# Optimization experiments

Measured on AMD Instinct MI355X. Metric: run time of the kernel, lower is better.

Reference implementation:

```python
import jax, jax.numpy as jnp
import numpy as np

SHAPE = 64
K = 8
HID = 512
OUT = K + 2 * K * SHAPE + 2 * SHAPE  # 1160
B, T = 32, 2048


def setup_inputs() -> dict:
    key = jax.random.key(0)
    ks = jax.random.split(key, 4)
    x = jax.random.normal(ks[0], (B, T, SHAPE), dtype=jnp.float32)
    W1 = jax.random.normal(ks[1], (SHAPE, HID), dtype=jnp.float32) / np.sqrt(SHAPE)
    b1 = jnp.zeros((HID,), dtype=jnp.float32)
    W2 = jax.random.normal(ks[2], (HID, HID), dtype=jnp.float32) / np.sqrt(HID)
    b2 = jnp.zeros((HID,), dtype=jnp.float32)
    W3 = jax.random.normal(ks[3], (HID, OUT), dtype=jnp.float32) / np.sqrt(HID) * 0.1
    b3 = jnp.zeros((OUT,), dtype=jnp.float32)
    return {"x": x, "W1": W1, "b1": b1, "W2": W2, "b2": b2, "W3": W3, "b3": b3}


def _coupling_forward(x, W1, b1, W2, b2, W3, b3):
    # coupling mask over feature dim: first half conditions the second half
    mask = jnp.zeros((SHAPE,), dtype=x.dtype).at[:SHAPE // 2].set(1.0)  # [D]
    x_ = x * mask  # [B,T,D]

    # conditioner MLP
    h = jax.nn.relu(x_ @ W1 + b1)
    h = jax.nn.relu(h @ W2 + b2)
    params = h @ W3 + b3  # [B,T,OUT]

    logscales = params[..., :SHAPE]
    biases = params[..., SHAPE:2 * SHAPE]
    mdn = params[..., 2 * SHAPE:]
    logits = mdn[..., :K]                                   # [B,T,K]
    mu = mdn[..., K:K + K * SHAPE].reshape(*x.shape[:2], K, SHAPE)
    logstd = mdn[..., K + K * SHAPE:].reshape(*x.shape[:2], K, SHAPE)

    # --- MixtureCDFFlow.flow ---
    weights = jax.nn.softmax(logits, axis=-1)[..., None]    # [B,T,K,1]
    std = jnp.exp(logstd)
    u = (x[:, :, None, :] - mu) / std                       # [B,T,K,D]
    cdf = 0.5 * (1.0 + jax.lax.erf(u / np.sqrt(2.0)))
    z = jnp.sum(cdf * weights, axis=2)                      # [B,T,D]
    pdf = jnp.exp(-0.5 * u * u) / (std * np.sqrt(2.0 * np.pi))
    logd_mix = jnp.log(jnp.sum(pdf * weights, axis=2))      # [B,T,D]

    # --- Inverse(Sigmoid).flow == Sigmoid.invert ---
    xs = -jnp.log(1.0 / z - 1.0)
    logd_sig = -jnp.log(z) - jnp.log(1.0 - z)

    # --- ElemwiseAffine.flow ---
    out = xs * jnp.exp(logscales) + biases
    log_det = logd_mix + logd_sig + logscales

    x_out = (1.0 - mask) * out + x_
    log_det = log_det * (1.0 - mask)
    return x_out, log_det


def reference(x, W1, b1, W2, b2, W3, b3):
    return _coupling_forward(x, W1, b1, W2, b2, W3, b3)
```

## Files before the change

kernel.cpp:

```cpp
#include <hip/hip_runtime.h>

typedef short short8 __attribute__((ext_vector_type(8)));
typedef float f32x4 __attribute__((ext_vector_type(4)));
typedef float f32x4v __attribute__((ext_vector_type(4)));

#define NROWS 65536
#define NCOMPACT 640

__device__ __forceinline__ short f2bf(float f) {
  union { float f; unsigned u; } c; c.f = f;
  unsigned r = (c.u + 0x7fffu + ((c.u >> 16) & 1u)) >> 16;
  return (short)r;
}

__device__ __forceinline__ float fastrcp(float a) {
  float r; asm("v_rcp_f32 %0, %1" : "=v"(r) : "v"(a)); return r;
}

__device__ __forceinline__ int w3col(int n) {
  if (n < 32)  return 32 + n;
  if (n < 64)  return 96 + (n - 32);
  if (n < 72)  return 128 + (n - 64);
  if (n < 96)  return -1;
  if (n < 352) { int q = n - 96;  return 168 + (q >> 5) * 64 + (q & 31); }
  if (n < 608) { int q = n - 352; return 680 + (q >> 5) * 64 + (q & 31); }
  return -1;
}

__global__ __launch_bounds__(256) void prep_w_kernel(
    const float* __restrict__ W1, const float* __restrict__ W2,
    const float* __restrict__ W3, const float* __restrict__ b3,
    short* __restrict__ w1t, short* __restrict__ w2t,
    short* __restrict__ w3t, float* __restrict__ b3c) {
  const int NW1 = 512 * 32, NW2 = 512 * 512, NW3 = NCOMPACT * 512;
  int t = blockIdx.x * 256 + threadIdx.x;
  if (t < NW1) {
    int n = t >> 5, k = t & 31;
    w1t[t] = f2bf(W1[k * 512 + n]);
  } else if (t < NW1 + NW2) {
    int i = t - NW1; int n = i >> 9, k = i & 511;
    w2t[i] = f2bf(W2[k * 512 + n]);
  } else if (t < NW1 + NW2 + NW3) {
    int i = t - NW1 - NW2; int n = i >> 9, k = i & 511;
    int c = w3col(n);
    w3t[i] = (c >= 0) ? f2bf(W3[(size_t)k * 1160 + c]) : (short)0;
  } else if (t < NW1 + NW2 + NW3 + NCOMPACT) {
    int n = t - NW1 - NW2 - NW3;
    int c = w3col(n);
    b3c[n] = (c >= 0) ? b3[c] : 0.0f;
  }
}

#define OFF_A 0
#define OFF_B 4096
#define OFF_C 45056
#define OFF_H 86016
#define PSTR 644

__global__ __launch_bounds__(1024) void mega_kernel(
    const float* __restrict__ x,
    const short* __restrict__ w1t,
    const float* __restrict__ b1,
    const short* __restrict__ w2t,
    const float* __restrict__ b2,
    const short* __restrict__ w3t,
    const float* __restrict__ b3c,
    float* __restrict__ out) {
  __shared__ __attribute__((aligned(16))) char lds[151552];
  const int tid = threadIdx.x;
  const int m0 = blockIdx.x * 64;
  const int lane = tid & 63, wid = tid >> 6;
  const int wr = wid >> 3, wc = wid & 7;
  const int lr = lane & 15, hi = lane >> 4, lk = hi * 8;
  short* Hs = (short*)(lds + OFF_H);

  auto STAGE_W = [&](int bo, const short* src, int stride, int kt, int nchunk) {
    for (int base = wid * 64; base < nchunk; base += 1024) {
      int c = base + lane;
      int row = c >> 2;
      int skb = ((c & 3) ^ ((row >> 1) & 3)) << 4;
      const char* g = (const char*)(src + (size_t)row * stride + kt) + skb;
      __builtin_amdgcn_global_load_lds(
          (const __attribute__((address_space(1))) void*)g,
          (__attribute__((address_space(3))) void*)(lds + bo + (size_t)base * 16),
          16, 0, 0);
    }
  };

  if (tid < 256) {
    int row = tid >> 2, seg = tid & 3;
    const float* src = x + (size_t)(m0 + row) * 64 + seg * 8;
    f32x4 v0 = *(const f32x4*)src;
    f32x4 v1 = *(const f32x4*)(src + 4);
    short8 v;
#pragma unroll
    for (int i = 0; i < 4; ++i) { v[i] = f2bf(v0[i]); v[4 + i] = f2bf(v1[i]); }
    int sseg = seg ^ ((row >> 1) & 3);
    *(short8*)(lds + OFF_A + row * 64 + sseg * 16) = v;
  }
  STAGE_W(OFF_B, w1t, 32, 0, 2048);
  __syncthreads();

  {
    const short* As = (const short*)(lds + OFF_A);
    const short* Ws = (const short*)(lds + OFF_B);
    f32x4 acc1[2][4] = {};
    short8 af[2];
#pragma unroll
    for (int mi = 0; mi < 2; ++mi) {
      int row = wr * 32 + mi * 16 + lr;
      af[mi] = *(const short8*)(&As[row * 32 + (lk ^ (((row >> 1) & 3) << 3))]);
    }
#pragma unroll
    for (int ni = 0; ni < 4; ++ni) {
      int brow = wc * 64 + ni * 16 + lr;
      short8 bf_ = *(const short8*)(&Ws[brow * 32 + (lk ^ (((brow >> 1) & 3) << 3))]);
      acc1[0][ni] = __builtin_amdgcn_mfma_f32_16x16x32_bf16(af[0], bf_, acc1[0][ni], 0, 0, 0);
      acc1[1][ni] = __builtin_amdgcn_mfma_f32_16x16x32_bf16(af[1], bf_, acc1[1][ni], 0, 0, 0);
    }
#pragma unroll
    for (int ni = 0; ni < 4; ++ni) {
      int col = wc * 64 + ni * 16 + lr;
      float bv = b1[col];
#pragma unroll
      for (int mi = 0; mi < 2; ++mi) {
#pragma unroll
        for (int j = 0; j < 4; ++j) {
          int row = wr * 32 + mi * 16 + hi * 4 + j;
          float v = fmaxf(acc1[mi][j >= 0 ? ni : ni][j] + bv, 0.0f);
          Hs[row * 512 + (col ^ ((row & 7) << 3))] = f2bf(v);
        }
      }
    }
  }
  STAGE_W(OFF_C, w2t, 512, 0, 2048);
  __syncthreads();

  {
    f32x4 acc2[2][4] = {};
    for (int t = 0; t < 16; ++t) {
      int buf  = (t & 1) ? OFF_B : OFF_C;
      if (t < 15) STAGE_W((t & 1) ? OFF_C : OFF_B, w2t, 512, (t + 1) * 32, 2048);
      const short* Ws = (const short*)(lds + buf);
      short8 af[2];
#pragma unroll
      for (int mi = 0; mi < 2; ++mi) {
        int row = wr * 32 + mi * 16 + lr;
        af[mi] = *(const short8*)(&Hs[row * 512 + ((t * 32 + lk) ^ ((row & 7) << 3))]);
      }
      __builtin_amdgcn_s_setprio(1);
#pragma unroll
      for (int ni = 0; ni < 4; ++ni) {
        int brow = wc * 64 + ni * 16 + lr;
        short8 bf_ = *(const short8*)(&Ws[brow * 32 + (lk ^ (((brow >> 1) & 3) << 3))]);
        acc2[0][ni] = __builtin_amdgcn_mfma_f32_16x16x32_bf16(af[0], bf_, acc2[0][ni], 0, 0, 0);
        acc2[1][ni] = __builtin_amdgcn_mfma_f32_16x16x32_bf16(af[1], bf_, acc2[1][ni], 0, 0, 0);
      }
      __builtin_amdgcn_s_setprio(0);
      __syncthreads();
    }
#pragma unroll
    for (int ni = 0; ni < 4; ++ni) {
      int col = wc * 64 + ni * 16 + lr;
      float bv = b2[col];
#pragma unroll
      for (int mi = 0; mi < 2; ++mi) {
#pragma unroll
        for (int j = 0; j < 4; ++j) {
          int row = wr * 32 + mi * 16 + hi * 4 + j;
          float v = fmaxf(acc2[mi][ni][j] + bv, 0.0f);
          Hs[row * 512 + (col ^ ((row & 7) << 3))] = f2bf(v);
        }
      }
    }
  }
  STAGE_W(OFF_C, w3t, 512, 0, 2560);
  __syncthreads();

  f32x4 acc3[2][5] = {};
  for (int t = 0; t < 16; ++t) {
    int buf = (t & 1) ? OFF_B : OFF_C;
    if (t < 15) STAGE_W((t & 1) ? OFF_C : OFF_B, w3t, 512, (t + 1) * 32, 2560);
    const short* Ws = (const short*)(lds + buf);
    short8 af[2];
#pragma unroll
    for (int mi = 0; mi < 2; ++mi) {
      int row = wr * 32 + mi * 16 + lr;
      af[mi] = *(const short8*)(&Hs[row * 512 + ((t * 32 + lk) ^ ((row & 7) << 3))]);
    }
    __builtin_amdgcn_s_setprio(1);
#pragma unroll
    for (int ni = 0; ni < 5; ++ni) {
      int brow = wc * 80 + ni * 16 + lr;
      short8 bf_ = *(const short8*)(&Ws[brow * 32 + (lk ^ (((brow >> 1) & 3) << 3))]);
      acc3[0][ni] = __builtin_amdgcn_mfma_f32_16x16x32_bf16(af[0], bf_, acc3[0][ni], 0, 0, 0);
      acc3[1][ni] = __builtin_amdgcn_mfma_f32_16x16x32_bf16(af[1], bf_, acc3[1][ni], 0, 0, 0);
    }
    __builtin_amdgcn_s_setprio(0);
    __syncthreads();
  }

  float* plds = (float*)lds;
  float* xo  = out;
  float* ldo = out + (size_t)NROWS * 64;
#pragma unroll
  for (int p = 0; p < 2; ++p) {
    if (p) __syncthreads();
    if (wr == p) {
#pragma unroll
      for (int mi2 = 0; mi2 < 2; ++mi2) {
#pragma unroll
        for (int ni = 0; ni < 5; ++ni) {
          int col = wc * 80 + ni * 16 + lr;
          float bv = b3c[col];
#pragma unroll
          for (int j = 0; j < 4; ++j)
            plds[(mi2 * 16 + hi * 4 + j) * PSTR + col] = acc3[mi2][ni][j] + bv;
        }
      }
    }
    __syncthreads();
    {
      int rl = tid >> 5, j = tid & 31;
      const float* p_ = plds + rl * PSTR;
      int grow = m0 + p * 32 + rl;

      float lg[8];
#pragma unroll
      for (int k = 0; k < 8; ++k) lg[k] = p_[64 + k];
      float mx = lg[0];
#pragma unroll
      for (int k = 1; k < 8; ++k) mx = fmaxf(mx, lg[k]);
      float wgt[8], wsum = 0.0f;
#pragma unroll
      for (int k = 0; k < 8; ++k) { wgt[k] = __expf(lg[k] - mx); wsum += wgt[k]; }

      float xd = x[(size_t)grow * 64 + 32 + j];
      float zs = 0.0f, ps = 0.0f;
#pragma unroll
      for (int k = 0; k < 8; ++k) {
        float mu   = p_[96 + k * 32 + j];
        float lstd = p_[352 + k * 32 + j];
        float istd = __expf(-lstd);
        float u = (xd - mu) * istd;
        float x2 = 0.5f * u * u;
        float e  = __expf(-x2);
        ps += wgt[k] * e * istd;
        float ax = fabsf(u) * 0.70710678118654752f;
        float t_ = fastrcp(fmaf(0.5f, ax, 1.0f));
        float poly = -1.26551223f + t_*(1.00002368f + t_*(0.37409196f +
                     t_*(0.09678418f + t_*(-0.18628806f + t_*(0.27886807f +
                     t_*(-1.13520398f + t_*(1.48851587f + t_*(-0.82215223f +
                     t_*0.17087277f))))))));
        float erfc_half = 0.5f * t_ * __expf(poly - x2);
        float cdf = (u >= 0.0f) ? 1.0f - erfc_half : erfc_half;
        zs += wgt[k] * cdf;
      }
      float winv = fastrcp(wsum);
      float z  = zs * winv;
      float pm = ps * winv * 0.39894228040143268f;
      float logz = __logf(z), log1mz = __logf(1.0f - z);
      float ls = p_[j], bv = p_[32 + j];
      float outv = (logz - log1mz) * __expf(ls) + bv;
      float ld = __logf(pm) - logz - log1mz + ls;

      size_t base = (size_t)grow * 64;
      xo[base + j]       = x[base + j];
      xo[base + 32 + j]  = outv;
      ldo[base + j]      = 0.0f;
      ldo[base + 32 + j] = ld;
    }
  }
}

extern "C" void kernel_launch(void* const* d_in, const int* in_sizes, int n_in,
                              void* d_out, int out_size, void* d_ws, size_t ws_size,
                              hipStream_t stream) {
  const float* x  = (const float*)d_in[0];
  const float* W1 = (const float*)d_in[1];
  const float* b1 = (const float*)d_in[2];
  const float* W2 = (const float*)d_in[3];
  const float* b2 = (const float*)d_in[4];
  const float* W3 = (const float*)d_in[5];
  const float* b3 = (const float*)d_in[6];
  char* ws = (char*)d_ws;

  short* w1t = (short*)ws;
  short* w2t = (short*)(ws + 32768);
  short* w3t = (short*)(ws + 557056);
  float* b3c = (float*)(ws + 1212416);
  float* out = (float*)d_out;

  {
    int total = 512 * 32 + 512 * 512 + NCOMPACT * 512 + NCOMPACT;
    prep_w_kernel<<<(total + 255) / 256, 256, 0, stream>>>(W1, W2, W3, b3, w1t, w2t, w3t, b3c);
  }
  mega_kernel<<<NROWS / 64, 1024, 0, stream>>>(x, w1t, b1, w2t, b2, w3t, b3c, out);
}
```

Baseline: 161.8 us.

## Load MLP weight fragments directly from global memory instead of LDS staging

Drops the double-buffered global_load_lds staging of W1/W2/W3 tiles. Each wave now reads its bf16 weight fragments straight from global memory, relying on the cache, and reads x directly into registers for the first layer. This removes the per-k-step __syncthreads and shrinks LDS from about 148KB to about 80KB, which may allow two 1024-thread blocks per CU. In exchange each weight tile is fetched by both row-group waves, through cache rather than shared LDS. The MFMA inner loops can also stall on global latency without explicit prefetch.

```diff
diff --git a/kernel.cpp b/kernel.cpp
--- a/kernel.cpp
+++ b/kernel.cpp
@@ -2,7 +2,6 @@
 
 typedef short short8 __attribute__((ext_vector_type(8)));
 typedef float f32x4 __attribute__((ext_vector_type(4)));
-typedef float f32x4v __attribute__((ext_vector_type(4)));
 
 #define NROWS 65536
 #define NCOMPACT 640
@@ -51,12 +50,7 @@
   }
 }
 
-#define OFF_A 0
-#define OFF_B 4096
-#define OFF_C 45056
-#define OFF_H 86016
 #define PSTR 644
-
 __global__ __launch_bounds__(1024) void mega_kernel(
     const float* __restrict__ x,
     const short* __restrict__ w1t,
@@ -66,55 +60,35 @@
     const short* __restrict__ w3t,
     const float* __restrict__ b3c,
     float* __restrict__ out) {
-  __shared__ __attribute__((aligned(16))) char lds[151552];
+  __shared__ __attribute__((aligned(16))) char lds[82432];
+  short* Hs = (short*)lds;
   const int tid = threadIdx.x;
   const int m0 = blockIdx.x * 64;
   const int lane = tid & 63, wid = tid >> 6;
   const int wr = wid >> 3, wc = wid & 7;
   const int lr = lane & 15, hi = lane >> 4, lk = hi * 8;
-  short* Hs = (short*)(lds + OFF_H);
-
-  auto STAGE_W = [&](int bo, const short* src, int stride, int kt, int nchunk) {
-    for (int base = wid * 64; base < nchunk; base += 1024) {
-      int c = base + lane;
-      int row = c >> 2;
-      int skb = ((c & 3) ^ ((row >> 1) & 3)) << 4;
-      const char* g = (const char*)(src + (size_t)row * stride + kt) + skb;
-      __builtin_amdgcn_global_load_lds(
-          (const __attribute__((address_space(1))) void*)g,
-          (__attribute__((address_space(3))) void*)(lds + bo + (size_t)base * 16),
-          16, 0, 0);
-    }
-  };
-
-  if (tid < 256) {
-    int row = tid >> 2, seg = tid & 3;
-    const float* src = x + (size_t)(m0 + row) * 64 + seg * 8;
-    f32x4 v0 = *(const f32x4*)src;
-    f32x4 v1 = *(const f32x4*)(src + 4);
-    short8 v;
-#pragma unroll
-    for (int i = 0; i < 4; ++i) { v[i] = f2bf(v0[i]); v[4 + i] = f2bf(v1[i]); }
-    int sseg = seg ^ ((row >> 1) & 3);
-    *(short8*)(lds + OFF_A + row * 64 + sseg * 16) = v;
-  }
-  STAGE_W(OFF_B, w1t, 32, 0, 2048);
-  __syncthreads();
-
-  {
-    const short* As = (const short*)(lds + OFF_A);
-    const short* Ws = (const short*)(lds + OFF_B);
-    f32x4 acc1[2][4] = {};
+
+  const int arow0 = wr * 32 + lr, arow1 = arow0 + 16;
+  const int asw0 = (arow0 & 7) << 3, asw1 = (arow1 & 7) << 3;
+
+  {
     short8 af[2];
 #pragma unroll
     for (int mi = 0; mi < 2; ++mi) {
       int row = wr * 32 + mi * 16 + lr;
-      af[mi] = *(const short8*)(&As[row * 32 + (lk ^ (((row >> 1) & 3) << 3))]);
-    }
+      const float* xs = x + (size_t)(m0 + row) * 64 + lk;
+      f32x4 v0 = *(const f32x4*)xs;
+      f32x4 v1 = *(const f32x4*)(xs + 4);
+      short8 v;
+#pragma unroll
+      for (int i = 0; i < 4; ++i) { v[i] = f2bf(v0[i]); v[4 + i] = f2bf(v1[i]); }
+      af[mi] = v;
+    }
+    f32x4 acc1[2][4] = {};
 #pragma unroll
     for (int ni = 0; ni < 4; ++ni) {
       int brow = wc * 64 + ni * 16 + lr;
-      short8 bf_ = *(const short8*)(&Ws[brow * 32 + (lk ^ (((brow >> 1) & 3) << 3))]);
+      short8 bf_ = *(const short8*)(w1t + brow * 32 + lk);
       acc1[0][ni] = __builtin_amdgcn_mfma_f32_16x16x32_bf16(af[0], bf_, acc1[0][ni], 0, 0, 0);
       acc1[1][ni] = __builtin_amdgcn_mfma_f32_16x16x32_bf16(af[1], bf_, acc1[1][ni], 0, 0, 0);
     }
@@ -123,82 +97,78 @@
       int col = wc * 64 + ni * 16 + lr;
       float bv = b1[col];
 #pragma unroll
-      for (int mi = 0; mi < 2; ++mi) {
+      for (int mi = 0; mi < 2; ++mi)
 #pragma unroll
         for (int j = 0; j < 4; ++j) {
           int row = wr * 32 + mi * 16 + hi * 4 + j;
-          float v = fmaxf(acc1[mi][j >= 0 ? ni : ni][j] + bv, 0.0f);
-          Hs[row * 512 + (col ^ ((row & 7) << 3))] = f2bf(v);
+          Hs[row * 512 + (col ^ ((row & 7) << 3))] =
+              f2bf(fmaxf(acc1[mi][ni][j] + bv, 0.0f));
         }
-      }
-    }
-  }
-  STAGE_W(OFF_C, w2t, 512, 0, 2048);
+    }
+  }
   __syncthreads();
 
   {
+    const short* p2[4];
+#pragma unroll
+    for (int ni = 0; ni < 4; ++ni)
+      p2[ni] = w2t + (size_t)(wc * 64 + ni * 16 + lr) * 512 + lk;
     f32x4 acc2[2][4] = {};
+#pragma unroll 2
     for (int t = 0; t < 16; ++t) {
-      int buf  = (t & 1) ? OFF_B : OFF_C;
-      if (t < 15) STAGE_W((t & 1) ? OFF_C : OFF_B, w2t, 512, (t + 1) * 32, 2048);
-      const short* Ws = (const short*)(lds + buf);
-      short8 af[2];
-#pragma unroll
-      for (int mi = 0; mi < 2; ++mi) {
-        int row = wr * 32 + mi * 16 + lr;
-        af[mi] = *(const short8*)(&Hs[row * 512 + ((t * 32 + lk) ^ ((row & 7) << 3))]);
-      }
+      short8 wf[4];
+#pragma unroll
+      for (int ni = 0; ni < 4; ++ni) wf[ni] = *(const short8*)(p2[ni] + t * 32);
+      short8 a0 = *(const short8*)(&Hs[arow0 * 512 + ((t * 32 + lk) ^ asw0)]);
+      short8 a1 = *(const short8*)(&Hs[arow1 * 512 + ((t * 32 + lk) ^ asw1)]);
       __builtin_amdgcn_s_setprio(1);
 #pragma unroll
       for (int ni = 0; ni < 4; ++ni) {
-        int brow = wc * 64 + ni * 16 + lr;
-        short8 bf_ = *(const short8*)(&Ws[brow * 32 + (lk ^ (((brow >> 1) & 3) << 3))]);
-        acc2[0][ni] = __builtin_amdgcn_mfma_f32_16x16x32_bf16(af[0], bf_, acc2[0][ni], 0, 0, 0);
-        acc2[1][ni] = __builtin_amdgcn_mfma_f32_16x16x32_bf16(af[1], bf_, acc2[1][ni], 0, 0, 0);
+        acc2[0][ni] = __builtin_amdgcn_mfma_f32_16x16x32_bf16(a0, wf[ni], acc2[0][ni], 0, 0, 0);
+        acc2[1][ni] = __builtin_amdgcn_mfma_f32_16x16x32_bf16(a1, wf[ni], acc2[1][ni], 0, 0, 0);
       }
       __builtin_amdgcn_s_setprio(0);
-      __syncthreads();
-    }
+    }
+    __syncthreads();
 #pragma unroll
     for (int ni = 0; ni < 4; ++ni) {
       int col = wc * 64 + ni * 16 + lr;
       float bv = b2[col];
 #pragma unroll
-      for (int mi = 0; mi < 2; ++mi) {
+      for (int mi = 0; mi < 2; ++mi)
 #pragma unroll
         for (int j = 0; j < 4; ++j) {
           int row = wr * 32 + mi * 16 + hi * 4 + j;
-          float v = fmaxf(acc2[mi][ni][j] + bv, 0.0f);
-          Hs[row * 512 + (col ^ ((row & 7) << 3))] = f2bf(v);
+          Hs[row * 512 + (col ^ ((row & 7) << 3))] =
+              f2bf(fmaxf(acc2[mi][ni][j] + bv, 0.0f));
         }
-      }
-    }
-  }
-  STAGE_W(OFF_C, w3t, 512, 0, 2560);
+    }
+  }
   __syncthreads();
 
   f32x4 acc3[2][5] = {};
-  for (int t = 0; t < 16; ++t) {
-    int buf = (t & 1) ? OFF_B : OFF_C;
-    if (t < 15) STAGE_W((t & 1) ? OFF_C : OFF_B, w3t, 512, (t + 1) * 32, 2560);
-    const short* Ws = (const short*)(lds + buf);
-    short8 af[2];
-#pragma unroll
-    for (int mi = 0; mi < 2; ++mi) {
-      int row = wr * 32 + mi * 16 + lr;
-      af[mi] = *(const short8*)(&Hs[row * 512 + ((t * 32 + lk) ^ ((row & 7) << 3))]);
-    }
-    __builtin_amdgcn_s_setprio(1);
-#pragma unroll
-    for (int ni = 0; ni < 5; ++ni) {
-      int brow = wc * 80 + ni * 16 + lr;
-      short8 bf_ = *(const short8*)(&Ws[brow * 32 + (lk ^ (((brow >> 1) & 3) << 3))]);
-      acc3[0][ni] = __builtin_amdgcn_mfma_f32_16x16x32_bf16(af[0], bf_, acc3[0][ni], 0, 0, 0);
-      acc3[1][ni] = __builtin_amdgcn_mfma_f32_16x16x32_bf16(af[1], bf_, acc3[1][ni], 0, 0, 0);
-    }
-    __builtin_amdgcn_s_setprio(0);
-    __syncthreads();
-  }
+  {
+    const short* p3[5];
+#pragma unroll
+    for (int ni = 0; ni < 5; ++ni)
+      p3[ni] = w3t + (size_t)(wc * 80 + ni * 16 + lr) * 512 + lk;
+#pragma unroll 2
+    for (int t = 0; t < 16; ++t) {
+      short8 wf[5];
+#pragma unroll
+      for (int ni = 0; ni < 5; ++ni) wf[ni] = *(const short8*)(p3[ni] + t * 32);
+      short8 a0 = *(const short8*)(&Hs[arow0 * 512 + ((t * 32 + lk) ^ asw0)]);
+      short8 a1 = *(const short8*)(&Hs[arow1 * 512 + ((t * 32 + lk) ^ asw1)]);
+      __builtin_amdgcn_s_setprio(1);
+#pragma unroll
+      for (int ni = 0; ni < 5; ++ni) {
+        acc3[0][ni] = __builtin_amdgcn_mfma_f32_16x16x32_bf16(a0, wf[ni], acc3[0][ni], 0, 0, 0);
+        acc3[1][ni] = __builtin_amdgcn_mfma_f32_16x16x32_bf16(a1, wf[ni], acc3[1][ni], 0, 0, 0);
+      }
+      __builtin_amdgcn_s_setprio(0);
+    }
+  }
+  __syncthreads();
 
   float* plds = (float*)lds;
   float* xo  = out;
```

Measured after the change: 314.1 us. 94.1% more time.
